# Optimization experiments

Measured on AMD Instinct MI355X. Metric: run time of the kernel, lower is better.

Reference implementation:

```python
import jax, jax.numpy as jnp
import numpy as np

N_HEADS = 12
ROPE_THETA = 10000.0


def _rope(x):
    # x: [B, L, N, D]; interleaved (lucidrains rotary_embedding_torch style) rotation over full D
    B, L, N, D = x.shape
    inv_freq = 1.0 / (ROPE_THETA ** (jnp.arange(0, D, 2, dtype=jnp.float32) / D))  # [D/2]
    freqs = jnp.arange(L, dtype=jnp.float32)[:, None] * inv_freq                    # [L, D/2]
    cos = jnp.repeat(jnp.cos(freqs), 2, axis=-1)[None, :, None, :].astype(x.dtype)  # [1,L,1,D]
    sin = jnp.repeat(jnp.sin(freqs), 2, axis=-1)[None, :, None, :].astype(x.dtype)
    x1 = x[..., 0::2]
    x2 = x[..., 1::2]
    x_rot = jnp.stack([-x2, x1], axis=-1).reshape(x.shape)  # rotate_half, interleaved pairs
    return x * cos + x_rot * sin


def setup_inputs() -> dict:
    key = jax.random.key(0)
    ks = jax.random.split(key, 7)
    B, L, dm = 8, 1024, 768
    x = jax.random.normal(ks[0], (B, L, dm), jnp.float32)
    mask = jax.random.randint(ks[1], (B, L), 0, 2, jnp.int32)          # 1 = keep, 0 = pad
    pos_bias = jax.random.normal(ks[2], (N_HEADS, L, L), jnp.float32) * 0.1
    qkv_w = jax.random.normal(ks[3], (3 * dm, dm), jnp.float32) * 0.02
    qkv_b = jax.random.normal(ks[4], (3 * dm,), jnp.float32) * 0.02
    out_w = jax.random.normal(ks[5], (dm, dm), jnp.float32) * 0.02
    out_b = jax.random.normal(ks[6], (dm,), jnp.float32) * 0.02
    return {"x": x, "pos_bias": pos_bias, "qkv_w": qkv_w, "qkv_b": qkv_b,
            "out_w": out_w, "out_b": out_b, "mask": mask}


def reference(x, pos_bias, qkv_w, qkv_b, out_w, out_b, mask):
    B, L, dm = x.shape
    N = N_HEADS
    D = dm // N
    # QKV projection (torch Linear: y = x @ W.T + b), chunk(3, -1)
    qkv = x @ qkv_w.T + qkv_b                                   # [B, L, 3*dm]
    q, k, v = [a.reshape(B, L, N, D) for a in jnp.split(qkv, 3, axis=-1)]
    q = _rope(q)
    k = _rope(k)
    # scores [B, N, Lq, Lk]
    scores = jnp.einsum('bqnd,bknd->bnqk', q, k) / jnp.sqrt(jnp.asarray(D, x.dtype))
    # mask_to_bias: (mask - 1) with negatives -> -inf, shape [B, 1, 1, L]
    mask_bias = jnp.where(mask > 0, 0.0, -jnp.inf).astype(x.dtype)[:, None, None, :]
    bias = pos_bias[None].astype(x.dtype) + mask_bias           # [B, N, L, L]
    attn = jax.nn.softmax(scores + bias, axis=-1)               # dropout = 0 (eval)
    o = jnp.einsum('bnqk,bknd->bqnd', attn, v).reshape(B, L, dm)
    return o @ out_w.T + out_b
```

## Files before the change

### kernel.cpp

```cpp
#include <hip/hip_runtime.h>

#define DEVINL __device__ __forceinline__

using bf16x8 = __attribute__((ext_vector_type(8))) short;
using f32x4  = __attribute__((ext_vector_type(4))) float;

constexpr int Bb = 8, Ls = 1024, DM = 768, NH = 12, DH = 64;
constexpr int QKV = 3 * DM;

DEVINL unsigned short f2bf(float f) {
    union { float f; unsigned u; } v; v.f = f;
    unsigned r = v.u + 0x7FFFu + ((v.u >> 16) & 1u);
    return (unsigned short)(r >> 16);
}
DEVINL float bf2f(unsigned short h) {
    union { unsigned u; float f; } v; v.u = ((unsigned)h) << 16; return v.f;
}

DEVINL void gload_lds16(const void* g, void* l) {
    __builtin_amdgcn_global_load_lds((const __attribute__((address_space(1))) void*)g,
                                     (__attribute__((address_space(3))) void*)l, 16, 0, 0);
}

__global__ void prep_kernel(const float* __restrict__ x, const float* __restrict__ wq,
                            const float* __restrict__ wo, const float* __restrict__ pbias,
                            unsigned short* __restrict__ xb, unsigned short* __restrict__ wqb,
                            unsigned short* __restrict__ wob, unsigned short* __restrict__ ebb,
                            float* __restrict__ tab) {
    const int X4 = Bb * Ls * DM / 4, W4 = QKV * DM / 4, O4 = DM * DM / 4;
    const int E4 = NH * Ls * Ls / 4, TB = Ls * DH;
    const int total = X4 + W4 + O4 + E4 + TB;
    const float L2E = 1.44269504089f;
    for (int idx = blockIdx.x * blockDim.x + threadIdx.x; idx < total;
         idx += gridDim.x * blockDim.x) {
        if (idx < X4 + W4 + O4) {
            const float4* s; unsigned short* d; int i;
            if (idx < X4)            { s = (const float4*)x;  d = xb;  i = idx; }
            else if (idx < X4 + W4)  { s = (const float4*)wq; d = wqb; i = idx - X4; }
            else                     { s = (const float4*)wo; d = wob; i = idx - X4 - W4; }
            float4 v = s[i];
            ushort4 o;
            o.x = f2bf(v.x); o.y = f2bf(v.y); o.z = f2bf(v.z); o.w = f2bf(v.w);
            ((ushort4*)d)[i] = o;
        } else if (idx < X4 + W4 + O4 + E4) {
            int i = idx - (X4 + W4 + O4);
            float4 v = ((const float4*)pbias)[i];
            ushort4 o;
            o.x = f2bf(v.x * L2E); o.y = f2bf(v.y * L2E);
            o.z = f2bf(v.z * L2E); o.w = f2bf(v.w * L2E);
            ((ushort4*)ebb)[i] = o;
        } else {
            int r = idx - (X4 + W4 + O4 + E4);
            int l = r >> 6, c = r & 63, i = c & 31;
            float freq = powf(10000.0f, -(float)i / 32.0f);
            float ang = (float)l * freq;
            tab[l * 64 + c] = (c < 32) ? cosf(ang) : sinf(ang);
        }
    }
}

template <int OUT_BF16>
__global__ __launch_bounds__(256) void gemm_nt(const unsigned short* __restrict__ A,
                                               const unsigned short* __restrict__ Bw,
                                               const float* __restrict__ bias,
                                               void* __restrict__ Cout,
                                               int M, int Nn, int K) {
    __shared__ unsigned short As[2][128 * 32];
    __shared__ unsigned short Bs[2][128 * 32];
    const int tid = threadIdx.x, lane = tid & 63, w = tid >> 6;
    const int f = blockIdx.x;
    const int bm = (8 * (f & 7) + ((f >> 3) & 7)) * 128;
    const int bn = (f >> 6) * 128;
    const int wm = w >> 1, wn = w & 1;
    const int col = lane & 15, q4 = lane >> 4;
    f32x4 acc[4][4] = {};

#define GSTAGE(bi, kt_)                                                              \
    {                                                                                \
        _Pragma("unroll") for (int i = 0; i < 2; ++i) {                              \
            int c0 = w * 128 + i * 64;                                               \
            int p = c0 + lane;                                                       \
            int row = p >> 2;                                                        \
            int kc = (p & 3) ^ (row & 3);                                            \
            gload_lds16(A + (size_t)(bm + row) * K + (kt_)*32 + kc * 8, &As[bi][c0 * 8]); \
            gload_lds16(Bw + (size_t)(bn + row) * K + (kt_)*32 + kc * 8, &Bs[bi][c0 * 8]); \
        }                                                                            \
    }

    const int NT = K / 32;
    GSTAGE(0, 0);
    for (int t = 0; t < NT; ++t) {
        const int cur = t & 1;
        if (t + 1 < NT) {
            GSTAGE(cur ^ 1, t + 1);
            asm volatile("s_waitcnt vmcnt(4)" ::: "memory");
        } else {
            asm volatile("s_waitcnt vmcnt(0)" ::: "memory");
        }
        __builtin_amdgcn_s_barrier();
        asm volatile("" ::: "memory");
        bf16x8 af[4], bfr[4];
#pragma unroll
        for (int tt = 0; tt < 4; ++tt) {
            int ra = wm * 64 + tt * 16 + col;
            int rb = wn * 64 + tt * 16 + col;
            af[tt]  = *(const bf16x8*)&As[cur][(ra * 32 + q4 * 8) ^ ((ra & 3) << 3)];
            bfr[tt] = *(const bf16x8*)&Bs[cur][(rb * 32 + q4 * 8) ^ ((rb & 3) << 3)];
        }
#pragma unroll
        for (int tt = 0; tt < 4; ++tt)
#pragma unroll
            for (int u = 0; u < 4; ++u)
                acc[tt][u] = __builtin_amdgcn_mfma_f32_16x16x32_bf16(af[tt], bfr[u], acc[tt][u], 0, 0, 0);
        __builtin_amdgcn_sched_barrier(0);
        asm volatile("" ::: "memory");
        __builtin_amdgcn_s_barrier();
    }
#undef GSTAGE
#pragma unroll
    for (int t = 0; t < 4; ++t) {
        int grow_base = bm + wm * 64 + t * 16 + q4 * 4;
#pragma unroll
        for (int u = 0; u < 4; ++u) {
            int gcol = bn + wn * 64 + u * 16 + col;
            float bv = bias[gcol];
#pragma unroll
            for (int r = 0; r < 4; ++r) {
                float vv = acc[t][u][r] + bv;
                if (OUT_BF16)
                    ((unsigned short*)Cout)[(size_t)(grow_base + r) * Nn + gcol] = f2bf(vv);
                else
                    ((float*)Cout)[(size_t)(grow_base + r) * Nn + gcol] = vv;
            }
        }
    }
}

__global__ void ropev_kernel(const unsigned short* __restrict__ qkvb, const float* __restrict__ tab,
                             unsigned short* __restrict__ qs, unsigned short* __restrict__ ks,
                             unsigned short* __restrict__ vt) {
    __shared__ unsigned short vsh[64][72];
    const int b = blockIdx.z, n = blockIdx.y, lt = blockIdx.x;
    const int tid = threadIdx.x;
    const float QSCL = 0.125f * 1.44269504089f;
#pragma unroll
    for (int i = 0; i < 2; ++i) {
        int idx = tid + i * 256;
        int l = lt * 64 + (idx >> 3), d8 = idx & 7;
        const unsigned short* src = qkvb + (size_t)(b * Ls + l) * QKV + n * DH + d8 * 8;
        float4 cs = *(const float4*)&tab[l * 64 + d8 * 4];
        float4 sn = *(const float4*)&tab[l * 64 + 32 + d8 * 4];
        float cv[4] = {cs.x, cs.y, cs.z, cs.w};
        float sv[4] = {sn.x, sn.y, sn.z, sn.w};
        size_t dsto = ((size_t)(b * NH + n) * Ls + l) * DH + d8 * 8;
        {
            bf16x8 qv = *(const bf16x8*)src;
            bf16x8 ov;
#pragma unroll
            for (int j = 0; j < 4; ++j) {
                float x1 = bf2f((unsigned short)qv[2 * j]), x2 = bf2f((unsigned short)qv[2 * j + 1]);
                ov[2 * j]     = (short)f2bf((x1 * cv[j] - x2 * sv[j]) * QSCL);
                ov[2 * j + 1] = (short)f2bf((x2 * cv[j] + x1 * sv[j]) * QSCL);
            }
            *(bf16x8*)(qs + dsto) = ov;
        }
        {
            bf16x8 kv = *(const bf16x8*)(src + DM);
            bf16x8 ov;
#pragma unroll
            for (int j = 0; j < 4; ++j) {
                float x1 = bf2f((unsigned short)kv[2 * j]), x2 = bf2f((unsigned short)kv[2 * j + 1]);
                ov[2 * j]     = (short)f2bf(x1 * cv[j] - x2 * sv[j]);
                ov[2 * j + 1] = (short)f2bf(x2 * cv[j] + x1 * sv[j]);
            }
            *(bf16x8*)(ks + dsto) = ov;
        }
    }
#pragma unroll
    for (int i = 0; i < 2; ++i) {
        int c = tid + i * 256;
        int lrow = c >> 3, d8 = c & 7;
        *(bf16x8*)&vsh[lrow][d8 * 8] =
            *(const bf16x8*)(qkvb + (size_t)(b * Ls + lt * 64 + lrow) * QKV + 2 * DM + n * DH + d8 * 8);
    }
    __syncthreads();
#pragma unroll
    for (int i = 0; i < 2; ++i) {
        int c = tid + i * 256;
        int d = c >> 3, l8 = c & 7;
        bf16x8 v;
#pragma unroll
        for (int j = 0; j < 8; ++j) v[j] = (short)vsh[l8 * 8 + j][d];
        *(bf16x8*)(vt + ((size_t)(b * NH + n) * DH + d) * Ls + lt * 64 + l8 * 8) = v;
    }
}

__global__ __launch_bounds__(256) void attn_kernel(const unsigned short* __restrict__ qs,
                                                   const unsigned short* __restrict__ ks,
                                                   const unsigned short* __restrict__ vt,
                                                   const unsigned short* __restrict__ ebb,
                                                   const int* __restrict__ mask,
                                                   unsigned short* __restrict__ ob) {
    __shared__ unsigned short Ksh[2][64 * 64];
    __shared__ unsigned short Vsh[2][64 * 64];
    __shared__ unsigned short EBsh[64 * 64];
    __shared__ unsigned short Psh[4][16 * 64];
    __shared__ float maskb[Ls];
    const int f = blockIdx.x;
    const int b = f / 192, t192 = f % 192;
    const int n = t192 % 12, qt = t192 / 12;
    const int tid = threadIdx.x, lane = tid & 63, w = tid >> 6;
    const int col = lane & 15, q4 = lane >> 4;
    for (int i = tid; i < Ls; i += 256)
        maskb[i] = (mask[b * Ls + i] > 0) ? 0.0f : -1e30f;
    const unsigned short* qbn = qs + (size_t)(b * NH + n) * Ls * DH;
    const unsigned short* kbn = ks + (size_t)(b * NH + n) * Ls * DH;
    const unsigned short* vbn = vt + (size_t)(b * NH + n) * DH * Ls;
    const unsigned short* ebn = ebb + (size_t)n * Ls * Ls;
    bf16x8 qf[2];
#pragma unroll
    for (int j = 0; j < 2; ++j)
        qf[j] = *(const bf16x8*)(qbn + (size_t)(qt * 64 + w * 16 + col) * DH + q4 * 8 + j * 32);
    float psum = 0.f;
    f32x4 oacc[4];
#pragma unroll
    for (int t = 0; t < 4; ++t) oacc[t] = f32x4{0.f, 0.f, 0.f, 0.f};
    __syncthreads();

#define STAGE_KV(bi, kt_)                                                                  \
    {                                                                                      \
        _Pragma("unroll") for (int i = 0; i < 2; ++i) {                                    \
            int c0 = w * 128 + i * 64;                                                     \
            int p = c0 + lane;                                                             \
            int row = p >> 3, cin = (p & 7) ^ (row & 7);                                   \
            gload_lds16(kbn + (size_t)((kt_)*64 + row) * DH + cin * 8, &Ksh[bi][c0 * 8]);  \
            gload_lds16(vbn + (size_t)row * Ls + (kt_)*64 + cin * 8, &Vsh[bi][c0 * 8]);    \
        }                                                                                  \
    }
#define STAGE_EB(kt_)                                                                      \
    {                                                                                      \
        _Pragma("unroll") for (int i = 0; i < 2; ++i) {                                    \
            int c0 = w * 128 + i * 64;                                                     \
            int p = c0 + lane;                                                             \
            int row = p >> 3, cin = (p & 7) ^ (row & 7);                                   \
            gload_lds16(ebn + (size_t)(qt * 64 + row) * Ls + (kt_)*64 + cin * 8, &EBsh[c0 * 8]); \
        }                                                                                  \
    }

    const int NT = Ls / 64;
    STAGE_KV(0, 0);
    STAGE_EB(0);
    for (int kt = 0; kt < NT; ++kt) {
        const int cur = kt & 1;
        if (kt + 1 < NT) {
            STAGE_KV(cur ^ 1, kt + 1);
            asm volatile("s_waitcnt vmcnt(4)" ::: "memory");
        } else {
            asm volatile("s_waitcnt vmcnt(0)" ::: "memory");
        }
        __builtin_amdgcn_s_barrier();
        asm volatile("" ::: "memory");
        f32x4 s[4];
#pragma unroll
        for (int t = 0; t < 4; ++t) {
            const f32x4 ma = *(const f32x4*)&maskb[kt * 64 + t * 16 + q4 * 4];
            ushort4 ebv = *(const ushort4*)&EBsh[(w * 16 + col) * 64 +
                                                (((t * 16 + q4 * 4)) ^ ((col & 7) << 3))];
            s[t][0] = bf2f(ebv.x) + ma[0];
            s[t][1] = bf2f(ebv.y) + ma[1];
            s[t][2] = bf2f(ebv.z) + ma[2];
            s[t][3] = bf2f(ebv.w) + ma[3];
        }
        __builtin_amdgcn_s_setprio(1);
#pragma unroll
        for (int t = 0; t < 4; ++t) {
            int krow = t * 16 + col;
#pragma unroll
            for (int j = 0; j < 2; ++j) {
                bf16x8 kf = *(const bf16x8*)&Ksh[cur][(krow * 64 + q4 * 8 + j * 32) ^ ((krow & 7) << 3)];
                s[t] = __builtin_amdgcn_mfma_f32_16x16x32_bf16(kf, qf[j], s[t], 0, 0, 0);
            }
        }
        __builtin_amdgcn_s_setprio(0);
        float p[4][4];
#pragma unroll
        for (int t = 0; t < 4; ++t)
#pragma unroll
            for (int r = 0; r < 4; ++r) {
                float pv = exp2f(s[t][r]);
                p[t][r] = pv;
                psum += pv;
            }
        asm volatile("s_waitcnt lgkmcnt(0)" ::: "memory");
        __builtin_amdgcn_sched_barrier(0);
        if (kt + 1 < NT) STAGE_EB(kt + 1);
        unsigned short* pw = Psh[w];
#pragma unroll
        for (int t = 0; t < 4; ++t) {
            unsigned pk0, pk1;
            asm("v_cvt_pk_bf16_f32 %0, %1, %2" : "=v"(pk0) : "v"(p[t][0]), "v"(p[t][1]));
            asm("v_cvt_pk_bf16_f32 %0, %1, %2" : "=v"(pk1) : "v"(p[t][2]), "v"(p[t][3]));
            uint2 pk; pk.x = pk0; pk.y = pk1;
            *(uint2*)&pw[(col * 64) + (((t * 16 + q4 * 4)) ^ ((col & 7) << 3))] = pk;
        }
        bf16x8 pa[2];
#pragma unroll
        for (int ksl = 0; ksl < 2; ++ksl)
            pa[ksl] = *(const bf16x8*)&pw[(col * 64) + ((ksl * 32 + q4 * 8) ^ ((col & 7) << 3))];
        __builtin_amdgcn_s_setprio(1);
#pragma unroll
        for (int ot = 0; ot < 4; ++ot) {
            int vrow = ot * 16 + col;
#pragma unroll
            for (int ksl = 0; ksl < 2; ++ksl) {
                bf16x8 vb = *(const bf16x8*)&Vsh[cur][(vrow * 64 + q4 * 8 + ksl * 32) ^ ((vrow & 7) << 3)];
                oacc[ot] = __builtin_amdgcn_mfma_f32_16x16x32_bf16(pa[ksl], vb, oacc[ot], 0, 0, 0);
            }
        }
        __builtin_amdgcn_s_setprio(0);
        __builtin_amdgcn_sched_barrier(0);
        asm volatile("" ::: "memory");
        __builtin_amdgcn_s_barrier();
    }
#undef STAGE_KV
#undef STAGE_EB
    psum += __shfl_xor(psum, 16);
    psum += __shfl_xor(psum, 32);
    float inv[4];
#pragma unroll
    for (int r = 0; r < 4; ++r)
        inv[r] = 1.0f / __shfl(psum, q4 * 4 + r);
#pragma unroll
    for (int r = 0; r < 4; ++r) {
        int lg = qt * 64 + w * 16 + q4 * 4 + r;
#pragma unroll
        for (int ot = 0; ot < 4; ++ot)
            ob[(size_t)(b * Ls + lg) * DM + n * DH + ot * 16 + col] = f2bf(oacc[ot][r] * inv[r]);
    }
}

extern "C" void kernel_launch(void* const* d_in, const int* in_sizes, int n_in,
                              void* d_out, int out_size, void* d_ws, size_t ws_size,
                              hipStream_t stream) {
    const float* x     = (const float*)d_in[0];
    const float* posb  = (const float*)d_in[1];
    const float* qkv_w = (const float*)d_in[2];
    const float* qkv_b = (const float*)d_in[3];
    const float* out_w = (const float*)d_in[4];
    const float* out_b = (const float*)d_in[5];
    const int*   mask  = (const int*)d_in[6];
    float* out = (float*)d_out;

    char* wp = (char*)d_ws;
    auto alloc = [&](size_t bytes) {
        char* p = wp;
        wp += (bytes + 255) & ~(size_t)255;
        return p;
    };
    unsigned short* xb   = (unsigned short*)alloc((size_t)Bb * Ls * DM * 2);
    unsigned short* wqb  = (unsigned short*)alloc((size_t)QKV * DM * 2);
    unsigned short* wob  = (unsigned short*)alloc((size_t)DM * DM * 2);
    unsigned short* ebb  = (unsigned short*)alloc((size_t)NH * Ls * Ls * 2);
    float*          tab  = (float*)alloc((size_t)Ls * DH * 4);
    unsigned short* qkvb = (unsigned short*)alloc((size_t)Bb * Ls * QKV * 2);
    unsigned short* qsb  = (unsigned short*)alloc((size_t)Bb * NH * Ls * DH * 2);
    unsigned short* ksb  = (unsigned short*)alloc((size_t)Bb * NH * Ls * DH * 2);
    unsigned short* vtb  = (unsigned short*)alloc((size_t)Bb * NH * DH * Ls * 2);
    unsigned short* obb  = (unsigned short*)alloc((size_t)Bb * Ls * DM * 2);

    prep_kernel<<<dim3(2048), dim3(256), 0, stream>>>(x, qkv_w, out_w, posb, xb, wqb, wob, ebb, tab);
    gemm_nt<1><<<dim3(1152), dim3(256), 0, stream>>>(xb, wqb, qkv_b, (void*)qkvb, Bb * Ls, QKV, DM);
    ropev_kernel<<<dim3(16, NH, Bb), dim3(256), 0, stream>>>(qkvb, tab, qsb, ksb, vtb);
    attn_kernel<<<dim3(1536), dim3(256), 0, stream>>>(qsb, ksb, vtb, ebb, mask, obb);
    gemm_nt<0><<<dim3(384), dim3(256), 0, stream>>>(obb, wob, out_b, (void*)out, Bb * Ls, DM, DM);
}
```

Baseline: 277.1 us.

## Fuse RoPE, Q scaling and V transpose into the QKV projection GEMM epilogue

```diff
diff --git a/kernel.cpp b/kernel.cpp
--- a/kernel.cpp
+++ b/kernel.cpp
@@ -51,12 +51,129 @@
             ((ushort4*)ebb)[i] = o;
         } else {
             int r = idx - (X4 + W4 + O4 + E4);
-            int l = r >> 6, c = r & 63, i = c & 31;
+            int l = r >> 6, c = r & 63, i = c >> 1;
             float freq = powf(10000.0f, -(float)i / 32.0f);
             float ang = (float)l * freq;
-            tab[l * 64 + c] = (c < 32) ? cosf(ang) : sinf(ang);
-        }
-    }
+            tab[l * 64 + c] = (c & 1) ? sinf(ang) : cosf(ang);
+        }
+    }
+}
+
+__global__ __launch_bounds__(256) void gemm_qkv(const unsigned short* __restrict__ A,
+                                                const unsigned short* __restrict__ Bw,
+                                                const float* __restrict__ bias,
+                                                const float* __restrict__ tab,
+                                                unsigned short* __restrict__ qs,
+                                                unsigned short* __restrict__ ks,
+                                                unsigned short* __restrict__ vt) {
+    constexpr int K = 768;
+    __shared__ unsigned short Sh[16384];
+#define ASP(bi) (Sh + (bi)*4096)
+#define BSP(bi) (Sh + 8192 + (bi)*4096)
+    const int tid = threadIdx.x, lane = tid & 63, w = tid >> 6;
+    const int f = blockIdx.x;
+    const int bm = (f % 18) * 128, bn = (f / 18) * 128;
+    const int wm = w >> 1, wn = w & 1;
+    const int col = lane & 15, q4 = lane >> 4;
+    f32x4 acc[4][4] = {};
+
+#define GSTAGE(bi, kt_)                                                                   \
+    {                                                                                     \
+        _Pragma("unroll") for (int i = 0; i < 2; ++i) {                                   \
+            int c0 = w * 128 + i * 64;                                                    \
+            int p = c0 + lane;                                                            \
+            int row = p >> 2;                                                             \
+            int kc = (p & 3) ^ (row & 3);                                                 \
+            gload_lds16(A + (size_t)(bm + row) * K + (kt_)*32 + kc * 8, ASP(bi) + c0 * 8);  \
+            gload_lds16(Bw + (size_t)(bn + row) * K + (kt_)*32 + kc * 8, BSP(bi) + c0 * 8); \
+        }                                                                                 \
+    }
+
+    const int NT = K / 32;
+    GSTAGE(0, 0);
+    for (int t = 0; t < NT; ++t) {
+        const int cur = t & 1;
+        if (t + 1 < NT) {
+            GSTAGE(cur ^ 1, t + 1);
+            asm volatile("s_waitcnt vmcnt(4)" ::: "memory");
+        } else {
+            asm volatile("s_waitcnt vmcnt(0)" ::: "memory");
+        }
+        __builtin_amdgcn_s_barrier();
+        asm volatile("" ::: "memory");
+        bf16x8 af[4], bfr[4];
+#pragma unroll
+        for (int tt = 0; tt < 4; ++tt) {
+            int ra = wm * 64 + tt * 16 + col;
+            int rb = wn * 64 + tt * 16 + col;
+            af[tt]  = *(const bf16x8*)&ASP(cur)[(ra * 32 + q4 * 8) ^ ((ra & 3) << 3)];
+            bfr[tt] = *(const bf16x8*)&BSP(cur)[(rb * 32 + q4 * 8) ^ ((rb & 3) << 3)];
+        }
+#pragma unroll
+        for (int tt = 0; tt < 4; ++tt)
+#pragma unroll
+            for (int u = 0; u < 4; ++u)
+                acc[tt][u] = __builtin_amdgcn_mfma_f32_16x16x32_bf16(af[tt], bfr[u], acc[tt][u], 0, 0, 0);
+        __builtin_amdgcn_sched_barrier(0);
+        asm volatile("" ::: "memory");
+        __builtin_amdgcn_s_barrier();
+    }
+#undef GSTAGE
+    __syncthreads();
+    unsigned short* tr = Sh + w * 4096;
+    const int btype = bm / 768;
+    const int n = ((bm % 768) + wm * 64) >> 6;
+    const float QS = (btype == 0) ? 0.125f * 1.44269504089f : 1.0f;
+#pragma unroll
+    for (int t = 0; t < 4; ++t) {
+        const int dloc = t * 16 + q4 * 4;
+        const int grow = bm + wm * 64 + dloc;
+        float bv[4];
+#pragma unroll
+        for (int r = 0; r < 4; ++r) bv[r] = bias[grow + r];
+#pragma unroll
+        for (int u = 0; u < 4; ++u) {
+            const int lt_ = u * 16 + col;
+            if (btype < 2) {
+                const int l = (bn + wn * 64 + lt_) & 1023;
+                float4 cs = *(const float4*)&tab[l * 64 + dloc];
+                float x0 = acc[t][u][0] + bv[0], x1 = acc[t][u][1] + bv[1];
+                float x2 = acc[t][u][2] + bv[2], x3 = acc[t][u][3] + bv[3];
+                ushort4 pk;
+                pk.x = f2bf((x0 * cs.x - x1 * cs.y) * QS);
+                pk.y = f2bf((x1 * cs.x + x0 * cs.y) * QS);
+                pk.z = f2bf((x2 * cs.z - x3 * cs.w) * QS);
+                pk.w = f2bf((x3 * cs.z + x2 * cs.w) * QS);
+                *(ushort4*)&tr[lt_ * 64 + (dloc ^ ((lt_ & 7) << 3))] = pk;
+            } else {
+#pragma unroll
+                for (int r = 0; r < 4; ++r) {
+                    int dr = dloc + r;
+                    tr[dr * 64 + (lt_ ^ ((dr & 7) << 3))] = f2bf(acc[t][u][r] + bv[r]);
+                }
+            }
+        }
+    }
+    asm volatile("s_waitcnt lgkmcnt(0)" ::: "memory");
+    __builtin_amdgcn_sched_barrier(0);
+    const int gt0 = bn + wn * 64;
+    const int b2 = gt0 >> 10;
+    if (btype < 2) {
+        const int l2 = (gt0 + lane) & 1023;
+        unsigned short* dstp = (btype ? ks : qs) + ((size_t)(b2 * NH + n) * Ls + l2) * DH;
+#pragma unroll
+        for (int c8 = 0; c8 < 8; ++c8)
+            *(bf16x8*)&dstp[c8 * 8] =
+                *(const bf16x8*)&tr[lane * 64 + ((c8 * 8) ^ ((lane & 7) << 3))];
+    } else {
+        unsigned short* dstp = vt + ((size_t)(b2 * NH + n) * DH + lane) * Ls + (gt0 & 1023);
+#pragma unroll
+        for (int c8 = 0; c8 < 8; ++c8)
+            *(bf16x8*)&dstp[c8 * 8] =
+                *(const bf16x8*)&tr[lane * 64 + ((c8 * 8) ^ ((lane & 7) << 3))];
+    }
+#undef ASP
+#undef BSP
 }
 
 template <int OUT_BF16>
@@ -133,65 +250,6 @@
                     ((float*)Cout)[(size_t)(grow_base + r) * Nn + gcol] = vv;
             }
         }
-    }
-}
-
-__global__ void ropev_kernel(const unsigned short* __restrict__ qkvb, const float* __restrict__ tab,
-                             unsigned short* __restrict__ qs, unsigned short* __restrict__ ks,
-                             unsigned short* __restrict__ vt) {
-    __shared__ unsigned short vsh[64][72];
-    const int b = blockIdx.z, n = blockIdx.y, lt = blockIdx.x;
-    const int tid = threadIdx.x;
-    const float QSCL = 0.125f * 1.44269504089f;
-#pragma unroll
-    for (int i = 0; i < 2; ++i) {
-        int idx = tid + i * 256;
-        int l = lt * 64 + (idx >> 3), d8 = idx & 7;
-        const unsigned short* src = qkvb + (size_t)(b * Ls + l) * QKV + n * DH + d8 * 8;
-        float4 cs = *(const float4*)&tab[l * 64 + d8 * 4];
-        float4 sn = *(const float4*)&tab[l * 64 + 32 + d8 * 4];
-        float cv[4] = {cs.x, cs.y, cs.z, cs.w};
-        float sv[4] = {sn.x, sn.y, sn.z, sn.w};
-        size_t dsto = ((size_t)(b * NH + n) * Ls + l) * DH + d8 * 8;
-        {
-            bf16x8 qv = *(const bf16x8*)src;
-            bf16x8 ov;
-#pragma unroll
-            for (int j = 0; j < 4; ++j) {
-                float x1 = bf2f((unsigned short)qv[2 * j]), x2 = bf2f((unsigned short)qv[2 * j + 1]);
-                ov[2 * j]     = (short)f2bf((x1 * cv[j] - x2 * sv[j]) * QSCL);
-                ov[2 * j + 1] = (short)f2bf((x2 * cv[j] + x1 * sv[j]) * QSCL);
-            }
-            *(bf16x8*)(qs + dsto) = ov;
-        }
-        {
-            bf16x8 kv = *(const bf16x8*)(src + DM);
-            bf16x8 ov;
-#pragma unroll
-            for (int j = 0; j < 4; ++j) {
-                float x1 = bf2f((unsigned short)kv[2 * j]), x2 = bf2f((unsigned short)kv[2 * j + 1]);
-                ov[2 * j]     = (short)f2bf(x1 * cv[j] - x2 * sv[j]);
-                ov[2 * j + 1] = (short)f2bf(x2 * cv[j] + x1 * sv[j]);
-            }
-            *(bf16x8*)(ks + dsto) = ov;
-        }
-    }
-#pragma unroll
-    for (int i = 0; i < 2; ++i) {
-        int c = tid + i * 256;
-        int lrow = c >> 3, d8 = c & 7;
-        *(bf16x8*)&vsh[lrow][d8 * 8] =
-            *(const bf16x8*)(qkvb + (size_t)(b * Ls + lt * 64 + lrow) * QKV + 2 * DM + n * DH + d8 * 8);
-    }
-    __syncthreads();
-#pragma unroll
-    for (int i = 0; i < 2; ++i) {
-        int c = tid + i * 256;
-        int d = c >> 3, l8 = c & 7;
-        bf16x8 v;
-#pragma unroll
-        for (int j = 0; j < 8; ++j) v[j] = (short)vsh[l8 * 8 + j][d];
-        *(bf16x8*)(vt + ((size_t)(b * NH + n) * DH + d) * Ls + lt * 64 + l8 * 8) = v;
     }
 }
 
@@ -362,15 +420,13 @@
     unsigned short* wob  = (unsigned short*)alloc((size_t)DM * DM * 2);
     unsigned short* ebb  = (unsigned short*)alloc((size_t)NH * Ls * Ls * 2);
     float*          tab  = (float*)alloc((size_t)Ls * DH * 4);
-    unsigned short* qkvb = (unsigned short*)alloc((size_t)Bb * Ls * QKV * 2);
     unsigned short* qsb  = (unsigned short*)alloc((size_t)Bb * NH * Ls * DH * 2);
     unsigned short* ksb  = (unsigned short*)alloc((size_t)Bb * NH * Ls * DH * 2);
     unsigned short* vtb  = (unsigned short*)alloc((size_t)Bb * NH * DH * Ls * 2);
     unsigned short* obb  = (unsigned short*)alloc((size_t)Bb * Ls * DM * 2);
 
     prep_kernel<<<dim3(2048), dim3(256), 0, stream>>>(x, qkv_w, out_w, posb, xb, wqb, wob, ebb, tab);
-    gemm_nt<1><<<dim3(1152), dim3(256), 0, stream>>>(xb, wqb, qkv_b, (void*)qkvb, Bb * Ls, QKV, DM);
-    ropev_kernel<<<dim3(16, NH, Bb), dim3(256), 0, stream>>>(qkvb, tab, qsb, ksb, vtb);
+    gemm_qkv<<<dim3(1152), dim3(256), 0, stream>>>(wqb, xb, qkv_b, tab, qsb, ksb, vtb);
     attn_kernel<<<dim3(1536), dim3(256), 0, stream>>>(qsb, ksb, vtb, ebb, mask, obb);
     gemm_nt<0><<<dim3(384), dim3(256), 0, stream>>>(obb, wob, out_b, (void*)out, Bb * Ls, DM, DM);
 }
```

Result: faster. 268.7 us (-3.0%).
